# Kernel optimization log

Measured on AMD Instinct MI355X. Metric: run time of the kernel, lower is better.

The kernel has to match this reference:

```python
import jax, jax.numpy as jnp
import numpy as np

B, DIM, N = 16, 512, 4096


def setup_inputs() -> dict:
    key = jax.random.key(0)
    kx, kq, kk, kv = jax.random.split(key, 4)
    scale = 1.0 / np.sqrt(DIM)
    return {
        "x": jax.random.normal(kx, (B, DIM, N), dtype=jnp.float32),
        "Wq": jax.random.normal(kq, (DIM, DIM), dtype=jnp.float32) * scale,
        "Wk": jax.random.normal(kk, (DIM, DIM), dtype=jnp.float32) * scale,
        "Wv": jax.random.normal(kv, (DIM, DIM), dtype=jnp.float32) * scale,
    }


def reference(x, Wq, Wk, Wv):
    # x: [B, dim, N]; 1x1 conv over channel dim == matmul with [dim_out, dim_in]
    dim = x.shape[1]
    temperature = jnp.sqrt(jnp.asarray(dim, dtype=x.dtype))
    q = jnp.einsum("dc,bcn->bdn", Wq, x)  # [B, dim, N]
    k = jnp.einsum("dc,bcn->bdn", Wk, x)
    v = jnp.einsum("dc,bcn->bdn", Wv, x)
    # channel attention: contract over N points -> [B, dim, dim]
    attn = jnp.einsum("bdn,ben->bde", q / temperature, k)
    attn = jax.nn.softmax(attn, axis=-1)
    out = jnp.einsum("bde,ben->bdn", attn, v)  # [B, dim, N]
    return out
```

## Files before the change

### kernel.cpp

```cpp
#include <hip/hip_runtime.h>
#include <hip/hip_bf16.h>
#include <math.h>

#define DIMC 512
#define NPT  4096
#define BATCH 16
#define KSPLIT 4

typedef __bf16 bf16x4 __attribute__((ext_vector_type(4)));
typedef __bf16 bf16x8 __attribute__((ext_vector_type(8)));
typedef float  f32x4  __attribute__((ext_vector_type(4)));

typedef const __attribute__((address_space(1))) unsigned int guint;
typedef __attribute__((address_space(3))) unsigned int luint;

__device__ inline void gl_lds16(const void* g, void* l) {
  __builtin_amdgcn_global_load_lds((guint*)g, (luint*)l, 16, 0, 0);
}

__global__ __launch_bounds__(256, 4) void gram_split(
    const __bf16* __restrict__ xb, float* __restrict__ Gp)
{
  static const int TI[10] = {0,0,0,0,1,1,1,2,2,3};
  static const int TJ[10] = {0,1,2,3,1,2,3,2,3,3};
  const int id = blockIdx.x;
  const int xcd = id & 7, slot = id >> 3;
  const int g = slot / 10, t = slot % 10;
  const int pair = xcd + 8 * g;
  const int b = pair >> 2, s = pair & 3;
  const int m0 = TI[t] * 128, n0 = TJ[t] * 128;

  const __bf16* A = xb + (long)b * DIMC * NPT;
  float* C = Gp + (long)pair * DIMC * DIMC;

  __shared__ alignas(16) __bf16 As[128 * 32];
  __shared__ alignas(16) __bf16 Bs[128 * 32];

  const int tid  = threadIdx.x;
  const int wave = tid >> 6, lane = tid & 63;
  const int wr = wave >> 1, wc = wave & 1;
  const int q = lane >> 4, p = lane & 15;
  const int r4 = lane >> 2;
  const int koff = (lane & 3) * 8;

  f32x4 acc[4][4];
#pragma unroll
  for (int i = 0; i < 4; ++i)
#pragma unroll
    for (int j = 0; j < 4; ++j) acc[i][j] = (f32x4){0.f, 0.f, 0.f, 0.f};

  const __bf16* gA = A + (long)m0 * NPT;
  const __bf16* gB = A + (long)n0 * NPT;
  const int kbeg = s * (NPT / KSPLIT), kend = kbeg + NPT / KSPLIT;

  for (int k0 = kbeg; k0 < kend; k0 += 32) {
    __syncthreads();
#pragma unroll
    for (int h = 0; h < 2; ++h) {
      const int chunk = wave + h * 4;
      gl_lds16(gA + (long)(chunk * 16 + r4) * NPT + k0 + koff, &As[chunk * 512]);
      gl_lds16(gB + (long)(chunk * 16 + r4) * NPT + k0 + koff, &Bs[chunk * 512]);
    }
    __syncthreads();

    bf16x8 af[4], bfv[4];
#pragma unroll
    for (int i = 0; i < 4; ++i)
      af[i] = ((const bf16x8*)As)[(wr * 64 + i * 16 + p) * 4 + q];
#pragma unroll
    for (int j = 0; j < 4; ++j)
      bfv[j] = ((const bf16x8*)Bs)[(wc * 64 + j * 16 + p) * 4 + q];
#pragma unroll
    for (int i = 0; i < 4; ++i)
#pragma unroll
      for (int j = 0; j < 4; ++j)
        acc[i][j] = __builtin_amdgcn_mfma_f32_16x16x32_bf16(af[i], bfv[j], acc[i][j], 0, 0, 0);
  }

#pragma unroll
  for (int i = 0; i < 4; ++i) {
    const int row = m0 + wr * 64 + i * 16 + q * 4;
#pragma unroll
    for (int j = 0; j < 4; ++j) {
      const int col = n0 + wc * 64 + j * 16 + p;
#pragma unroll
      for (int r = 0; r < 4; ++r)
        C[(long)(row + r) * DIMC + col] = acc[i][j][r];
    }
  }
}

__global__ __launch_bounds__(256) void gram_reduce_mirror(
    const float* __restrict__ Gp, __bf16* __restrict__ Gh, __bf16* __restrict__ Gl)
{
  const int bid = blockIdx.x;
  const int b = bid / 36;
  int rem = bid % 36, I = 0;
  while (rem >= 8 - I) { rem -= 8 - I; ++I; }
  const int J = I + rem;

  __shared__ float T[64][65];
  const int tid = threadIdx.x;
  const int r = tid >> 2, c0 = (tid & 3) * 16;

  float v[16];
#pragma unroll
  for (int e = 0; e < 16; ++e) v[e] = 0.f;
#pragma unroll
  for (int s = 0; s < KSPLIT; ++s) {
    const float* src = Gp + (long)(b * KSPLIT + s) * DIMC * DIMC
                          + (long)(I * 64 + r) * DIMC + J * 64 + c0;
#pragma unroll
    for (int q = 0; q < 4; ++q) {
      float4 t4 = ((const float4*)src)[q];
      v[q * 4 + 0] += t4.x; v[q * 4 + 1] += t4.y;
      v[q * 4 + 2] += t4.z; v[q * 4 + 3] += t4.w;
    }
  }

  const long gbase = (long)b * DIMC * DIMC;
#pragma unroll
  for (int q = 0; q < 4; ++q) {
    bf16x4 h, l;
#pragma unroll
    for (int e = 0; e < 4; ++e) {
      float f = v[q * 4 + e];
      __bf16 hh = (__bf16)f;
      h[e] = hh; l[e] = (__bf16)(f - (float)hh);
    }
    const long o = gbase + (long)(I * 64 + r) * DIMC + J * 64 + c0 + q * 4;
    *(bf16x4*)(Gh + o) = h;
    *(bf16x4*)(Gl + o) = l;
  }
#pragma unroll
  for (int e = 0; e < 16; ++e) T[r][c0 + e] = v[e];
  __syncthreads();
  if (I != J) {
#pragma unroll
    for (int q = 0; q < 4; ++q) {
      bf16x4 h, l;
#pragma unroll
      for (int e = 0; e < 4; ++e) {
        float f = T[c0 + q * 4 + e][r];
        __bf16 hh = (__bf16)f;
        h[e] = hh; l[e] = (__bf16)(f - (float)hh);
      }
      const long o = gbase + (long)(J * 64 + r) * DIMC + I * 64 + c0 + q * 4;
      *(bf16x4*)(Gh + o) = h;
      *(bf16x4*)(Gl + o) = l;
    }
  }
}

template <bool SPLIT_OUT>
__global__ __launch_bounds__(256, 4) void gemm3_nt(
    const __bf16* __restrict__ Ah, const __bf16* __restrict__ Al,
    const __bf16* __restrict__ Bh, const __bf16* __restrict__ Bl,
    float* __restrict__ Cf, __bf16* __restrict__ Ch, __bf16* __restrict__ Cl,
    int K, long sA, long sB, long sC, float alpha)
{
  const int b = blockIdx.z;
  Ah += (long)b * sA;  Al += (long)b * sA;
  Bh += (long)b * sB;  Bl += (long)b * sB;
  const int m0 = blockIdx.y * 64, n0 = blockIdx.x * 128;

  __shared__ alignas(16) __bf16 sAh[64 * 32],  sAl[64 * 32];
  __shared__ alignas(16) __bf16 sBh[128 * 32], sBl[128 * 32];

  const int tid  = threadIdx.x;
  const int wave = tid >> 6, lane = tid & 63;
  const int wr = wave >> 1, wc = wave & 1;
  const int q = lane >> 4, p = lane & 15;
  const int r4 = lane >> 2;
  const int koff = (lane & 3) * 8;

  f32x4 acc[2][4];
#pragma unroll
  for (int i = 0; i < 2; ++i)
#pragma unroll
    for (int j = 0; j < 4; ++j) acc[i][j] = (f32x4){0.f, 0.f, 0.f, 0.f};

  const long arow = (long)(m0 + wave * 16 + r4) * K + koff;

  for (int k0 = 0; k0 < K; k0 += 32) {
    __syncthreads();
    gl_lds16(Ah + arow + k0, &sAh[wave * 512]);
    gl_lds16(Al + arow + k0, &sAl[wave * 512]);
#pragma unroll
    for (int h = 0; h < 2; ++h) {
      const int chunk = wave + h * 4;
      const long brow = (long)(n0 + chunk * 16 + r4) * K + koff + k0;
      gl_lds16(Bh + brow, &sBh[chunk * 512]);
      gl_lds16(Bl + brow, &sBl[chunk * 512]);
    }
    __syncthreads();

    bf16x8 fah[2], fal[2], fbh[4], fbl[4];
#pragma unroll
    for (int i = 0; i < 2; ++i) {
      const int idx = (wr * 32 + i * 16 + p) * 4 + q;
      fah[i] = ((const bf16x8*)sAh)[idx];
      fal[i] = ((const bf16x8*)sAl)[idx];
    }
#pragma unroll
    for (int j = 0; j < 4; ++j) {
      const int idx = (wc * 64 + j * 16 + p) * 4 + q;
      fbh[j] = ((const bf16x8*)sBh)[idx];
      fbl[j] = ((const bf16x8*)sBl)[idx];
    }
#pragma unroll
    for (int i = 0; i < 2; ++i)
#pragma unroll
      for (int j = 0; j < 4; ++j) {
        acc[i][j] = __builtin_amdgcn_mfma_f32_16x16x32_bf16(fah[i], fbh[j], acc[i][j], 0, 0, 0);
        acc[i][j] = __builtin_amdgcn_mfma_f32_16x16x32_bf16(fah[i], fbl[j], acc[i][j], 0, 0, 0);
        acc[i][j] = __builtin_amdgcn_mfma_f32_16x16x32_bf16(fal[i], fbh[j], acc[i][j], 0, 0, 0);
      }
  }

#pragma unroll
  for (int i = 0; i < 2; ++i) {
    const int row = m0 + wr * 32 + i * 16 + q * 4;
#pragma unroll
    for (int j = 0; j < 4; ++j) {
      const int col = n0 + wc * 64 + j * 16 + p;
#pragma unroll
      for (int r = 0; r < 4; ++r) {
        const float f = acc[i][j][r] * alpha;
        const long o = (long)b * sC + (long)(row + r) * DIMC + col;
        if (SPLIT_OUT) {
          __bf16 hh = (__bf16)f;
          Ch[o] = hh;
          Cl[o] = (__bf16)(f - (float)hh);
        } else {
          Cf[o] = f;
        }
      }
    }
  }
}

__global__ __launch_bounds__(256, 4) void gemm_nt64x128(
    const __bf16* __restrict__ A, const __bf16* __restrict__ B,
    __bf16* __restrict__ C, int K, long sA, long sB, long sC)
{
  const int b = blockIdx.z;
  A += (long)b * sA;  B += (long)b * sB;  C += (long)b * sC;
  const int m0 = blockIdx.y * 64, n0 = blockIdx.x * 128;

  __shared__ alignas(16) __bf16 As[64 * 32];
  __shared__ alignas(16) __bf16 Bs[128 * 32];

  const int tid  = threadIdx.x;
  const int wave = tid >> 6, lane = tid & 63;
  const int wr = wave >> 1, wc = wave & 1;
  const int q = lane >> 4, p = lane & 15;
  const int r4 = lane >> 2;
  const int koff = (lane & 3) * 8;

  f32x4 acc[2][4];
#pragma unroll
  for (int i = 0; i < 2; ++i)
#pragma unroll
    for (int j = 0; j < 4; ++j) acc[i][j] = (f32x4){0.f, 0.f, 0.f, 0.f};

  const long arow = (long)(m0 + wave * 16 + r4) * K + koff;

  for (int k0 = 0; k0 < K; k0 += 32) {
    __syncthreads();
    gl_lds16(A + arow + k0, &As[wave * 512]);
#pragma unroll
    for (int h = 0; h < 2; ++h) {
      const int chunk = wave + h * 4;
      gl_lds16(B + (long)(n0 + chunk * 16 + r4) * K + koff + k0, &Bs[chunk * 512]);
    }
    __syncthreads();

    bf16x8 af[2], bfv[4];
#pragma unroll
    for (int i = 0; i < 2; ++i)
      af[i] = ((const bf16x8*)As)[(wr * 32 + i * 16 + p) * 4 + q];
#pragma unroll
    for (int j = 0; j < 4; ++j)
      bfv[j] = ((const bf16x8*)Bs)[(wc * 64 + j * 16 + p) * 4 + q];
#pragma unroll
    for (int i = 0; i < 2; ++i)
#pragma unroll
      for (int j = 0; j < 4; ++j)
        acc[i][j] = __builtin_amdgcn_mfma_f32_16x16x32_bf16(af[i], bfv[j], acc[i][j], 0, 0, 0);
  }

#pragma unroll
  for (int i = 0; i < 2; ++i) {
    const int row = m0 + wr * 32 + i * 16 + q * 4;
#pragma unroll
    for (int j = 0; j < 4; ++j) {
      const int col = n0 + wc * 64 + j * 16 + p;
#pragma unroll
      for (int r = 0; r < 4; ++r)
        C[(long)(row + r) * DIMC + col] = (__bf16)acc[i][j][r];
    }
  }
}

__global__ __launch_bounds__(256, 3) void gemm_final(
    const __bf16* __restrict__ Mm, const __bf16* __restrict__ xb,
    float* __restrict__ out)
{
  const int id = blockIdx.x;
  const int xcd = id & 7, slot = id >> 3;
  const int g = slot >> 7, tile = slot & 127;
  const int b = xcd + 8 * g;
  const int m0 = (tile >> 5) * 128, n0 = (tile & 31) * 128;

  const __bf16* A = Mm + (long)b * DIMC * DIMC;
  const __bf16* B = xb + (long)b * DIMC * NPT;
  float* C = out + (long)b * DIMC * NPT;
  const int K = DIMC;

  __shared__ alignas(16) __bf16 As[2][128 * 32];
  __shared__ alignas(16) unsigned int Bs[2][128 * 18];

  const int tid  = threadIdx.x;
  const int wave = tid >> 6, lane = tid & 63;
  const int wr = wave >> 1, wc = wave & 1;
  const int q = lane >> 4, p = lane & 15;
  const int r4 = lane >> 2;
  const int koff = (lane & 3) * 8;

  const int ng = tid & 31;
  const int cq = tid >> 5;

  f32x4 acc[4][4];
#pragma unroll
  for (int i = 0; i < 4; ++i)
#pragma unroll
    for (int j = 0; j < 4; ++j) acc[i][j] = (f32x4){0.f, 0.f, 0.f, 0.f};

  const __bf16* gA = A + (long)m0 * K;
  const __bf16* gBrow = B + n0 + ng * 4;

  auto stage_a = [&](int k0, int buf) {
#pragma unroll
    for (int h = 0; h < 2; ++h) {
      const int chunk = wave + h * 4;
      gl_lds16(gA + (long)(chunk * 16 + r4) * K + k0 + koff, &As[buf][chunk * 512]);
    }
  };
  auto load_b = [&](int k0, uint2* rd) {
#pragma unroll
    for (int r = 0; r < 4; ++r)
      rd[r] = *(const uint2*)(gBrow + (long)(k0 + cq * 4 + r) * NPT);
  };
  auto pack_b = [&](const uint2* rd, int buf) {
#pragma unroll
    for (int nn = 0; nn < 4; ++nn) {
      const unsigned int s0 = (nn < 2) ? rd[0].x : rd[0].y;
      const unsigned int s1 = (nn < 2) ? rd[1].x : rd[1].y;
      const unsigned int s2 = (nn < 2) ? rd[2].x : rd[2].y;
      const unsigned int s3 = (nn < 2) ? rd[3].x : rd[3].y;
      unsigned int o01, o23;
      if (nn & 1) {
        o01 = (s0 >> 16) | (s1 & 0xffff0000u);
        o23 = (s2 >> 16) | (s3 & 0xffff0000u);
      } else {
        o01 = (s0 & 0xffffu) | (s1 << 16);
        o23 = (s2 & 0xffffu) | (s3 << 16);
      }
      uint2 o; o.x = o01; o.y = o23;
      *(uint2*)&Bs[buf][(ng * 4 + nn) * 18 + cq * 2] = o;
    }
  };

  {
    stage_a(0, 0);
    uint2 rd[4];
    load_b(0, rd);
    pack_b(rd, 0);
  }
  __syncthreads();

  int cur = 0;
  for (int k0 = 0; k0 < K; k0 += 32) {
    const int nxt = cur ^ 1;
    const bool more = (k0 + 32) < K;
    uint2 rd[4];
    if (more) {
      stage_a(k0 + 32, nxt);
      load_b(k0 + 32, rd);
    }

    bf16x8 af[4], bfv[4];
#pragma unroll
    for (int i = 0; i < 4; ++i)
      af[i] = ((const bf16x8*)As[cur])[(wr * 64 + i * 16 + p) * 4 + q];
#pragma unroll
    for (int j = 0; j < 4; ++j) {
      const unsigned int* bp = &Bs[cur][(wc * 64 + j * 16 + p) * 18 + q * 4];
      const uint2 lo = *(const uint2*)bp;
      const uint2 hi = *(const uint2*)(bp + 2);
      union { uint4 u; bf16x8 v; } cvt;
      cvt.u.x = lo.x; cvt.u.y = lo.y; cvt.u.z = hi.x; cvt.u.w = hi.y;
      bfv[j] = cvt.v;
    }
#pragma unroll
    for (int i = 0; i < 4; ++i)
#pragma unroll
      for (int j = 0; j < 4; ++j)
        acc[i][j] = __builtin_amdgcn_mfma_f32_16x16x32_bf16(af[i], bfv[j], acc[i][j], 0, 0, 0);

    if (more) pack_b(rd, nxt);
    __syncthreads();
    cur = nxt;
  }

#pragma unroll
  for (int i = 0; i < 4; ++i) {
    const int row = m0 + wr * 64 + i * 16 + q * 4;
#pragma unroll
    for (int j = 0; j < 4; ++j) {
      const int col = n0 + wc * 64 + j * 16 + p;
#pragma unroll
      for (int r = 0; r < 4; ++r)
        C[(long)(row + r) * NPT + col] = acc[i][j][r];
    }
  }
}

__global__ __launch_bounds__(256) void softmax_rows(
    const float* __restrict__ S, __bf16* __restrict__ P)
{
  const int row = blockIdx.x * 4 + (threadIdx.x >> 6);
  const int lane = threadIdx.x & 63;
  const float4* s4 = (const float4*)(S + (long)row * DIMC);
  float4 a = s4[lane * 2], b = s4[lane * 2 + 1];
  float v[8] = {a.x, a.y, a.z, a.w, b.x, b.y, b.z, b.w};
  float m = v[0];
#pragma unroll
  for (int i = 1; i < 8; ++i) m = fmaxf(m, v[i]);
#pragma unroll
  for (int off = 32; off > 0; off >>= 1) m = fmaxf(m, __shfl_xor(m, off));
  float e[8], sum = 0.f;
#pragma unroll
  for (int i = 0; i < 8; ++i) { e[i] = expf(v[i] - m); sum += e[i]; }
#pragma unroll
  for (int off = 32; off > 0; off >>= 1) sum += __shfl_xor(sum, off);
  const float inv = 1.0f / sum;
  bf16x8 o;
#pragma unroll
  for (int i = 0; i < 8; ++i) o[i] = (__bf16)(e[i] * inv);
  ((bf16x8*)(P + (long)row * DIMC))[lane] = o;
}

__global__ __launch_bounds__(256) void prep(
    const float* __restrict__ x, __bf16* __restrict__ xb,
    const float* __restrict__ Wq, const float* __restrict__ Wk,
    const float* __restrict__ Wv,
    __bf16* __restrict__ Wqh, __bf16* __restrict__ Wql,
    __bf16* __restrict__ Wkh, __bf16* __restrict__ Wkl,
    __bf16* __restrict__ WvT)
{
  if (blockIdx.x < 1024) {
    const int i = blockIdx.x * 256 + threadIdx.x;
    float q = Wq[i];
    __bf16 qh = (__bf16)q; Wqh[i] = qh; Wql[i] = (__bf16)(q - (float)qh);
    float k = Wk[i];
    __bf16 kh = (__bf16)k; Wkh[i] = kh; Wkl[i] = (__bf16)(k - (float)kh);
    const int e = i >> 9, c = i & 511;
    WvT[(long)c * DIMC + e] = (__bf16)Wv[i];
    return;
  }
  const long total8 = (long)BATCH * DIMC * NPT / 8;
  const long stride = (long)(gridDim.x - 1024) * 256;
  for (long i = (long)(blockIdx.x - 1024) * 256 + threadIdx.x; i < total8; i += stride) {
    const f32x4 a = ((const f32x4*)x)[2 * i];
    const f32x4 b = ((const f32x4*)x)[2 * i + 1];
    bf16x8 o;
    o[0] = (__bf16)a[0]; o[1] = (__bf16)a[1];
    o[2] = (__bf16)a[2]; o[3] = (__bf16)a[3];
    o[4] = (__bf16)b[0]; o[5] = (__bf16)b[1];
    o[6] = (__bf16)b[2]; o[7] = (__bf16)b[3];
    ((bf16x8*)xb)[i] = o;
  }
}

extern "C" void kernel_launch(void* const* d_in, const int* in_sizes, int n_in,
                              void* d_out, int out_size, void* d_ws, size_t ws_size,
                              hipStream_t stream)
{
  const float* x  = (const float*)d_in[0];
  const float* Wq = (const float*)d_in[1];
  const float* Wk = (const float*)d_in[2];
  const float* Wv = (const float*)d_in[3];
  float* out = (float*)d_out;

  char* ws = (char*)d_ws;
  size_t off = 0;
  auto alloc = [&](size_t bytes) -> void* {
    void* p = ws + off;
    off += (bytes + 255) & ~(size_t)255;
    return p;
  };
  const long s2 = (long)DIMC * DIMC;

  __bf16* xb  = (__bf16*)alloc((size_t)BATCH * DIMC * NPT * 2);
  float*  Gp  = (float*) alloc((size_t)KSPLIT * BATCH * s2 * 4);
  __bf16* Gh  = (__bf16*)alloc((size_t)BATCH * s2 * 2);
  __bf16* Gl  = (__bf16*)alloc((size_t)BATCH * s2 * 2);
  __bf16* Hh  = (__bf16*)alloc((size_t)BATCH * s2 * 2);
  __bf16* Hl  = (__bf16*)alloc((size_t)BATCH * s2 * 2);
  __bf16* Wqh = (__bf16*)alloc((size_t)s2 * 2);
  __bf16* Wql = (__bf16*)alloc((size_t)s2 * 2);
  __bf16* Wkh = (__bf16*)alloc((size_t)s2 * 2);
  __bf16* Wkl = (__bf16*)alloc((size_t)s2 * 2);
  __bf16* WvT = (__bf16*)alloc((size_t)s2 * 2);
  float*  S  = (float*)Gp;
  __bf16* P  = Gl;
  __bf16* Mm = Gh;

  prep<<<3072, 256, 0, stream>>>(x, xb, Wq, Wk, Wv, Wqh, Wql, Wkh, Wkl, WvT);
  gram_split<<<640, 256, 0, stream>>>(xb, Gp);
  gram_reduce_mirror<<<BATCH * 36, 256, 0, stream>>>(Gp, Gh, Gl);
  gemm3_nt<true><<<dim3(4, 8, BATCH), 256, 0, stream>>>(
      Wqh, Wql, Gh, Gl, (float*)nullptr, Hh, Hl, DIMC, 0L, s2, s2, 1.0f);
  gemm3_nt<false><<<dim3(4, 8, BATCH), 256, 0, stream>>>(
      Hh, Hl, Wkh, Wkl, S, (__bf16*)nullptr, (__bf16*)nullptr,
      DIMC, s2, 0L, s2, 0.044194173824159216f);
  softmax_rows<<<BATCH * DIMC / 4, 256, 0, stream>>>(S, P);
  gemm_nt64x128<<<dim3(4, 8, BATCH), 256, 0, stream>>>(
      P, WvT, Mm, DIMC, s2, 0L, s2);
  gemm_final<<<2048, 256, 0, stream>>>(Mm, xb, out);
}
```

Baseline: 394.2 us.

## Double K-tile depth to 64 with XOR-swizzled LDS layout across GEMM kernels

```diff
diff --git a/kernel.cpp b/kernel.cpp
--- a/kernel.cpp
+++ b/kernel.cpp
@@ -18,7 +18,8 @@
   __builtin_amdgcn_global_load_lds((guint*)g, (luint*)l, 16, 0, 0);
 }
 
-__global__ __launch_bounds__(256, 4) void gram_split(
+
+__global__ __launch_bounds__(256, 3) void gram_split(
     const __bf16* __restrict__ xb, float* __restrict__ Gp)
 {
   static const int TI[10] = {0,0,0,0,1,1,1,2,2,3};
@@ -33,15 +34,16 @@
   const __bf16* A = xb + (long)b * DIMC * NPT;
   float* C = Gp + (long)pair * DIMC * DIMC;
 
-  __shared__ alignas(16) __bf16 As[128 * 32];
-  __shared__ alignas(16) __bf16 Bs[128 * 32];
+  __shared__ alignas(16) __bf16 As[128 * 64];
+  __shared__ alignas(16) __bf16 Bs[128 * 64];
 
   const int tid  = threadIdx.x;
   const int wave = tid >> 6, lane = tid & 63;
   const int wr = wave >> 1, wc = wave & 1;
   const int q = lane >> 4, p = lane & 15;
-  const int r4 = lane >> 2;
-  const int koff = (lane & 3) * 8;
+  const int r8 = lane >> 3;
+  const int sk8 = (((lane & 7) ^ (r8 & 7)) * 8);
+  const int px = p & 7;
 
   f32x4 acc[4][4];
 #pragma unroll
@@ -53,28 +55,31 @@
   const __bf16* gB = A + (long)n0 * NPT;
   const int kbeg = s * (NPT / KSPLIT), kend = kbeg + NPT / KSPLIT;
 
-  for (int k0 = kbeg; k0 < kend; k0 += 32) {
-    __syncthreads();
-#pragma unroll
-    for (int h = 0; h < 2; ++h) {
+  for (int k0 = kbeg; k0 < kend; k0 += 64) {
+    __syncthreads();
+#pragma unroll
+    for (int h = 0; h < 4; ++h) {
       const int chunk = wave + h * 4;
-      gl_lds16(gA + (long)(chunk * 16 + r4) * NPT + k0 + koff, &As[chunk * 512]);
-      gl_lds16(gB + (long)(chunk * 16 + r4) * NPT + k0 + koff, &Bs[chunk * 512]);
-    }
-    __syncthreads();
-
-    bf16x8 af[4], bfv[4];
-#pragma unroll
-    for (int i = 0; i < 4; ++i)
-      af[i] = ((const bf16x8*)As)[(wr * 64 + i * 16 + p) * 4 + q];
-#pragma unroll
-    for (int j = 0; j < 4; ++j)
-      bfv[j] = ((const bf16x8*)Bs)[(wc * 64 + j * 16 + p) * 4 + q];
-#pragma unroll
-    for (int i = 0; i < 4; ++i)
+      gl_lds16(gA + (long)(chunk * 8 + r8) * NPT + k0 + sk8, &As[chunk * 512]);
+      gl_lds16(gB + (long)(chunk * 8 + r8) * NPT + k0 + sk8, &Bs[chunk * 512]);
+    }
+    __syncthreads();
+
+#pragma unroll
+    for (int kk = 0; kk < 2; ++kk) {
+      bf16x8 af[4], bfv[4];
+#pragma unroll
+      for (int i = 0; i < 4; ++i)
+        af[i] = ((const bf16x8*)As)[(wr * 64 + i * 16 + p) * 8 + ((kk * 4 + q) ^ px)];
 #pragma unroll
       for (int j = 0; j < 4; ++j)
-        acc[i][j] = __builtin_amdgcn_mfma_f32_16x16x32_bf16(af[i], bfv[j], acc[i][j], 0, 0, 0);
+        bfv[j] = ((const bf16x8*)Bs)[(wc * 64 + j * 16 + p) * 8 + ((kk * 4 + q) ^ px)];
+#pragma unroll
+      for (int i = 0; i < 4; ++i)
+#pragma unroll
+        for (int j = 0; j < 4; ++j)
+          acc[i][j] = __builtin_amdgcn_mfma_f32_16x16x32_bf16(af[i], bfv[j], acc[i][j], 0, 0, 0);
+    }
   }
 
 #pragma unroll
@@ -153,7 +158,7 @@
 }
 
 template <bool SPLIT_OUT>
-__global__ __launch_bounds__(256, 4) void gemm3_nt(
+__global__ __launch_bounds__(256, 2) void gemm3_nt(
     const __bf16* __restrict__ Ah, const __bf16* __restrict__ Al,
     const __bf16* __restrict__ Bh, const __bf16* __restrict__ Bl,
     float* __restrict__ Cf, __bf16* __restrict__ Ch, __bf16* __restrict__ Cl,
@@ -164,15 +169,16 @@
   Bh += (long)b * sB;  Bl += (long)b * sB;
   const int m0 = blockIdx.y * 64, n0 = blockIdx.x * 128;
 
-  __shared__ alignas(16) __bf16 sAh[64 * 32],  sAl[64 * 32];
-  __shared__ alignas(16) __bf16 sBh[128 * 32], sBl[128 * 32];
+  __shared__ alignas(16) __bf16 sAh[64 * 64],  sAl[64 * 64];
+  __shared__ alignas(16) __bf16 sBh[128 * 64], sBl[128 * 64];
 
   const int tid  = threadIdx.x;
   const int wave = tid >> 6, lane = tid & 63;
   const int wr = wave >> 1, wc = wave & 1;
   const int q = lane >> 4, p = lane & 15;
-  const int r4 = lane >> 2;
-  const int koff = (lane & 3) * 8;
+  const int r8 = lane >> 3;
+  const int sk8 = (((lane & 7) ^ (r8 & 7)) * 8);
+  const int px = p & 7;
 
   f32x4 acc[2][4];
 #pragma unroll
@@ -180,42 +186,48 @@
 #pragma unroll
     for (int j = 0; j < 4; ++j) acc[i][j] = (f32x4){0.f, 0.f, 0.f, 0.f};
 
-  const long arow = (long)(m0 + wave * 16 + r4) * K + koff;
-
-  for (int k0 = 0; k0 < K; k0 += 32) {
-    __syncthreads();
-    gl_lds16(Ah + arow + k0, &sAh[wave * 512]);
-    gl_lds16(Al + arow + k0, &sAl[wave * 512]);
+  for (int k0 = 0; k0 < K; k0 += 64) {
+    __syncthreads();
 #pragma unroll
     for (int h = 0; h < 2; ++h) {
       const int chunk = wave + h * 4;
-      const long brow = (long)(n0 + chunk * 16 + r4) * K + koff + k0;
+      const long arow = (long)(m0 + chunk * 8 + r8) * K + k0 + sk8;
+      gl_lds16(Ah + arow, &sAh[chunk * 512]);
+      gl_lds16(Al + arow, &sAl[chunk * 512]);
+    }
+#pragma unroll
+    for (int h = 0; h < 4; ++h) {
+      const int chunk = wave + h * 4;
+      const long brow = (long)(n0 + chunk * 8 + r8) * K + k0 + sk8;
       gl_lds16(Bh + brow, &sBh[chunk * 512]);
       gl_lds16(Bl + brow, &sBl[chunk * 512]);
     }
     __syncthreads();
 
-    bf16x8 fah[2], fal[2], fbh[4], fbl[4];
-#pragma unroll
-    for (int i = 0; i < 2; ++i) {
-      const int idx = (wr * 32 + i * 16 + p) * 4 + q;
-      fah[i] = ((const bf16x8*)sAh)[idx];
-      fal[i] = ((const bf16x8*)sAl)[idx];
-    }
-#pragma unroll
-    for (int j = 0; j < 4; ++j) {
-      const int idx = (wc * 64 + j * 16 + p) * 4 + q;
-      fbh[j] = ((const bf16x8*)sBh)[idx];
-      fbl[j] = ((const bf16x8*)sBl)[idx];
-    }
-#pragma unroll
-    for (int i = 0; i < 2; ++i)
+#pragma unroll
+    for (int kk = 0; kk < 2; ++kk) {
+      bf16x8 fah[2], fal[2], fbh[4], fbl[4];
+#pragma unroll
+      for (int i = 0; i < 2; ++i) {
+        const int idx = (wr * 32 + i * 16 + p) * 8 + ((kk * 4 + q) ^ px);
+        fah[i] = ((const bf16x8*)sAh)[idx];
+        fal[i] = ((const bf16x8*)sAl)[idx];
+      }
 #pragma unroll
       for (int j = 0; j < 4; ++j) {
-        acc[i][j] = __builtin_amdgcn_mfma_f32_16x16x32_bf16(fah[i], fbh[j], acc[i][j], 0, 0, 0);
-        acc[i][j] = __builtin_amdgcn_mfma_f32_16x16x32_bf16(fah[i], fbl[j], acc[i][j], 0, 0, 0);
-        acc[i][j] = __builtin_amdgcn_mfma_f32_16x16x32_bf16(fal[i], fbh[j], acc[i][j], 0, 0, 0);
+        const int idx = (wc * 64 + j * 16 + p) * 8 + ((kk * 4 + q) ^ px);
+        fbh[j] = ((const bf16x8*)sBh)[idx];
+        fbl[j] = ((const bf16x8*)sBl)[idx];
       }
+#pragma unroll
+      for (int i = 0; i < 2; ++i)
+#pragma unroll
+        for (int j = 0; j < 4; ++j) {
+          acc[i][j] = __builtin_amdgcn_mfma_f32_16x16x32_bf16(fah[i], fbh[j], acc[i][j], 0, 0, 0);
+          acc[i][j] = __builtin_amdgcn_mfma_f32_16x16x32_bf16(fah[i], fbl[j], acc[i][j], 0, 0, 0);
+          acc[i][j] = __builtin_amdgcn_mfma_f32_16x16x32_bf16(fal[i], fbh[j], acc[i][j], 0, 0, 0);
+        }
+    }
   }
 
 #pragma unroll
@@ -240,7 +252,7 @@
   }
 }
 
-__global__ __launch_bounds__(256, 4) void gemm_nt64x128(
+__global__ __launch_bounds__(256, 2) void gemm_nt64x128(
     const __bf16* __restrict__ A, const __bf16* __restrict__ B,
     __bf16* __restrict__ C, int K, long sA, long sB, long sC)
 {
@@ -248,15 +260,16 @@
   A += (long)b * sA;  B += (long)b * sB;  C += (long)b * sC;
   const int m0 = blockIdx.y * 64, n0 = blockIdx.x * 128;
 
-  __shared__ alignas(16) __bf16 As[64 * 32];
-  __shared__ alignas(16) __bf16 Bs[128 * 32];
+  __shared__ alignas(16) __bf16 As[64 * 64];
+  __shared__ alignas(16) __bf16 Bs[128 * 64];
 
   const int tid  = threadIdx.x;
   const int wave = tid >> 6, lane = tid & 63;
   const int wr = wave >> 1, wc = wave & 1;
   const int q = lane >> 4, p = lane & 15;
-  const int r4 = lane >> 2;
-  const int koff = (lane & 3) * 8;
+  const int r8 = lane >> 3;
+  const int sk8 = (((lane & 7) ^ (r8 & 7)) * 8);
+  const int px = p & 7;
 
   f32x4 acc[2][4];
 #pragma unroll
@@ -264,30 +277,35 @@
 #pragma unroll
     for (int j = 0; j < 4; ++j) acc[i][j] = (f32x4){0.f, 0.f, 0.f, 0.f};
 
-  const long arow = (long)(m0 + wave * 16 + r4) * K + koff;
-
-  for (int k0 = 0; k0 < K; k0 += 32) {
-    __syncthreads();
-    gl_lds16(A + arow + k0, &As[wave * 512]);
+  for (int k0 = 0; k0 < K; k0 += 64) {
+    __syncthreads();
 #pragma unroll
     for (int h = 0; h < 2; ++h) {
       const int chunk = wave + h * 4;
-      gl_lds16(B + (long)(n0 + chunk * 16 + r4) * K + koff + k0, &Bs[chunk * 512]);
-    }
-    __syncthreads();
-
-    bf16x8 af[2], bfv[4];
-#pragma unroll
-    for (int i = 0; i < 2; ++i)
-      af[i] = ((const bf16x8*)As)[(wr * 32 + i * 16 + p) * 4 + q];
-#pragma unroll
-    for (int j = 0; j < 4; ++j)
-      bfv[j] = ((const bf16x8*)Bs)[(wc * 64 + j * 16 + p) * 4 + q];
-#pragma unroll
-    for (int i = 0; i < 2; ++i)
+      gl_lds16(A + (long)(m0 + chunk * 8 + r8) * K + k0 + sk8, &As[chunk * 512]);
+    }
+#pragma unroll
+    for (int h = 0; h < 4; ++h) {
+      const int chunk = wave + h * 4;
+      gl_lds16(B + (long)(n0 + chunk * 8 + r8) * K + k0 + sk8, &Bs[chunk * 512]);
+    }
+    __syncthreads();
+
+#pragma unroll
+    for (int kk = 0; kk < 2; ++kk) {
+      bf16x8 af[2], bfv[4];
+#pragma unroll
+      for (int i = 0; i < 2; ++i)
+        af[i] = ((const bf16x8*)As)[(wr * 32 + i * 16 + p) * 8 + ((kk * 4 + q) ^ px)];
 #pragma unroll
       for (int j = 0; j < 4; ++j)
-        acc[i][j] = __builtin_amdgcn_mfma_f32_16x16x32_bf16(af[i], bfv[j], acc[i][j], 0, 0, 0);
+        bfv[j] = ((const bf16x8*)Bs)[(wc * 64 + j * 16 + p) * 8 + ((kk * 4 + q) ^ px)];
+#pragma unroll
+      for (int i = 0; i < 2; ++i)
+#pragma unroll
+        for (int j = 0; j < 4; ++j)
+          acc[i][j] = __builtin_amdgcn_mfma_f32_16x16x32_bf16(af[i], bfv[j], acc[i][j], 0, 0, 0);
+    }
   }
 
 #pragma unroll
@@ -318,18 +336,19 @@
   float* C = out + (long)b * DIMC * NPT;
   const int K = DIMC;
 
-  __shared__ alignas(16) __bf16 As[2][128 * 32];
-  __shared__ alignas(16) unsigned int Bs[2][128 * 18];
+  __shared__ alignas(16) __bf16 As[128 * 64];
+  __shared__ alignas(16) unsigned int Bs[128 * 34];
 
   const int tid  = threadIdx.x;
   const int wave = tid >> 6, lane = tid & 63;
   const int wr = wave >> 1, wc = wave & 1;
   const int q = lane >> 4, p = lane & 15;
-  const int r4 = lane >> 2;
-  const int koff = (lane & 3) * 8;
+  const int r8 = lane >> 3;
+  const int sk8 = (((lane & 7) ^ (r8 & 7)) * 8);
+  const int px = p & 7;
 
   const int ng = tid & 31;
-  const int cq = tid >> 5;
+  const int cg = tid >> 5;
 
   f32x4 acc[4][4];
 #pragma unroll
@@ -340,78 +359,59 @@
   const __bf16* gA = A + (long)m0 * K;
   const __bf16* gBrow = B + n0 + ng * 4;
 
-  auto stage_a = [&](int k0, int buf) {
-#pragma unroll
-    for (int h = 0; h < 2; ++h) {
+  for (int k0 = 0; k0 < K; k0 += 64) {
+    __syncthreads();
+#pragma unroll
+    for (int h = 0; h < 4; ++h) {
       const int chunk = wave + h * 4;
-      gl_lds16(gA + (long)(chunk * 16 + r4) * K + k0 + koff, &As[buf][chunk * 512]);
-    }
-  };
-  auto load_b = [&](int k0, uint2* rd) {
-#pragma unroll
-    for (int r = 0; r < 4; ++r)
-      rd[r] = *(const uint2*)(gBrow + (long)(k0 + cq * 4 + r) * NPT);
-  };
-  auto pack_b = [&](const uint2* rd, int buf) {
+      gl_lds16(gA + (long)(chunk * 8 + r8) * K + k0 + sk8, &As[chunk * 512]);
+    }
+    uint2 rd[8];
+#pragma unroll
+    for (int r = 0; r < 8; ++r)
+      rd[r] = *(const uint2*)(gBrow + (long)(k0 + cg * 8 + r) * NPT);
 #pragma unroll
     for (int nn = 0; nn < 4; ++nn) {
-      const unsigned int s0 = (nn < 2) ? rd[0].x : rd[0].y;
-      const unsigned int s1 = (nn < 2) ? rd[1].x : rd[1].y;
-      const unsigned int s2 = (nn < 2) ? rd[2].x : rd[2].y;
-      const unsigned int s3 = (nn < 2) ? rd[3].x : rd[3].y;
-      unsigned int o01, o23;
-      if (nn & 1) {
-        o01 = (s0 >> 16) | (s1 & 0xffff0000u);
-        o23 = (s2 >> 16) | (s3 & 0xffff0000u);
-      } else {
-        o01 = (s0 & 0xffffu) | (s1 << 16);
-        o23 = (s2 & 0xffffu) | (s3 << 16);
+      unsigned int s[8];
+#pragma unroll
+      for (int r = 0; r < 8; ++r) s[r] = (nn < 2) ? rd[r].x : rd[r].y;
+      unsigned int dw[4];
+#pragma unroll
+      for (int t = 0; t < 4; ++t) {
+        if (nn & 1)
+          dw[t] = (s[2 * t] >> 16) | (s[2 * t + 1] & 0xffff0000u);
+        else
+          dw[t] = (s[2 * t] & 0xffffu) | (s[2 * t + 1] << 16);
       }
-      uint2 o; o.x = o01; o.y = o23;
-      *(uint2*)&Bs[buf][(ng * 4 + nn) * 18 + cq * 2] = o;
-    }
-  };
-
-  {
-    stage_a(0, 0);
-    uint2 rd[4];
-    load_b(0, rd);
-    pack_b(rd, 0);
-  }
-  __syncthreads();
-
-  int cur = 0;
-  for (int k0 = 0; k0 < K; k0 += 32) {
-    const int nxt = cur ^ 1;
-    const bool more = (k0 + 32) < K;
-    uint2 rd[4];
-    if (more) {
-      stage_a(k0 + 32, nxt);
-      load_b(k0 + 32, rd);
-    }
-
-    bf16x8 af[4], bfv[4];
-#pragma unroll
-    for (int i = 0; i < 4; ++i)
-      af[i] = ((const bf16x8*)As[cur])[(wr * 64 + i * 16 + p) * 4 + q];
-#pragma unroll
-    for (int j = 0; j < 4; ++j) {
-      const unsigned int* bp = &Bs[cur][(wc * 64 + j * 16 + p) * 18 + q * 4];
-      const uint2 lo = *(const uint2*)bp;
-      const uint2 hi = *(const uint2*)(bp + 2);
-      union { uint4 u; bf16x8 v; } cvt;
-      cvt.u.x = lo.x; cvt.u.y = lo.y; cvt.u.z = hi.x; cvt.u.w = hi.y;
-      bfv[j] = cvt.v;
-    }
-#pragma unroll
-    for (int i = 0; i < 4; ++i)
-#pragma unroll
-      for (int j = 0; j < 4; ++j)
-        acc[i][j] = __builtin_amdgcn_mfma_f32_16x16x32_bf16(af[i], bfv[j], acc[i][j], 0, 0, 0);
-
-    if (more) pack_b(rd, nxt);
-    __syncthreads();
-    cur = nxt;
+      unsigned int* bp = &Bs[(ng * 4 + nn) * 34 + cg * 4];
+      uint2 o0; o0.x = dw[0]; o0.y = dw[1];
+      uint2 o1; o1.x = dw[2]; o1.y = dw[3];
+      *(uint2*)bp = o0;
+      *(uint2*)(bp + 2) = o1;
+    }
+    __syncthreads();
+
+#pragma unroll
+    for (int kk = 0; kk < 2; ++kk) {
+      bf16x8 af[4], bfv[4];
+#pragma unroll
+      for (int i = 0; i < 4; ++i)
+        af[i] = ((const bf16x8*)As)[(wr * 64 + i * 16 + p) * 8 + ((kk * 4 + q) ^ px)];
+#pragma unroll
+      for (int j = 0; j < 4; ++j) {
+        const unsigned int* bp = &Bs[(wc * 64 + j * 16 + p) * 34 + kk * 16 + q * 4];
+        const uint2 lo = *(const uint2*)bp;
+        const uint2 hi = *(const uint2*)(bp + 2);
+        union { uint4 u; bf16x8 v; } cvt;
+        cvt.u.x = lo.x; cvt.u.y = lo.y; cvt.u.z = hi.x; cvt.u.w = hi.y;
+        bfv[j] = cvt.v;
+      }
+#pragma unroll
+      for (int i = 0; i < 4; ++i)
+#pragma unroll
+        for (int j = 0; j < 4; ++j)
+          acc[i][j] = __builtin_amdgcn_mfma_f32_16x16x32_bf16(af[i], bfv[j], acc[i][j], 0, 0, 0);
+    }
   }
 
 #pragma unroll
```

After: 378.4 us. -4.0%, faster.
